# Optimization experiments

Hardware: AMD Instinct MI355X
Metric: run time of the kernel (lower is better)

## Reference

```python
import jax, jax.numpy as jnp
import numpy as np
from jax import lax

B, C, H, W = 4, 192, 64, 64
D_STATE, D_CONV, EXPAND = 16, 4, 2
D_INNER = EXPAND * C           # 384
DT_RANK = (C + 15) // 16       # 12 (mamba_ssm default ceil(d_model/16))


def setup_inputs() -> dict:
    key = jax.random.key(0)
    ks = jax.random.split(key, 12)
    sc = lambda k, shape, s=0.02: (jax.random.normal(k, shape, jnp.float32) * s)
    x = jax.random.normal(ks[0], (B, C, H, W), jnp.float32)
    norm_w = jnp.ones((C,), jnp.float32)
    norm_b = jnp.zeros((C,), jnp.float32)
    in_proj_w = sc(ks[1], (2 * D_INNER, C))
    conv_w = sc(ks[2], (D_INNER, D_CONV), 0.1)
    conv_b = jnp.zeros((D_INNER,), jnp.float32)
    x_proj_w = sc(ks[3], (DT_RANK + 2 * D_STATE, D_INNER))
    dt_proj_w = sc(ks[4], (D_INNER, DT_RANK), 0.1)
    # dt bias init so softplus(dt_bias) is in a realistic [1e-3, 1e-1] range
    dt0 = jax.random.uniform(ks[5], (D_INNER,), jnp.float32, 0.001, 0.1)
    dt_proj_b = jnp.log(jnp.expm1(dt0))
    A_log = jnp.log(jnp.broadcast_to(
        jnp.arange(1, D_STATE + 1, dtype=jnp.float32), (D_INNER, D_STATE)))
    D = jnp.ones((D_INNER,), jnp.float32)
    out_proj_w = sc(ks[6], (C, D_INNER))
    return {"x": x, "norm_w": norm_w, "norm_b": norm_b, "in_proj_w": in_proj_w,
            "conv_w": conv_w, "conv_b": conv_b, "x_proj_w": x_proj_w,
            "dt_proj_w": dt_proj_w, "dt_proj_b": dt_proj_b, "A_log": A_log,
            "D": D, "out_proj_w": out_proj_w}


def _mamba2d(x, norm_w, norm_b, in_proj_w, conv_w, conv_b, x_proj_w,
             dt_proj_w, dt_proj_b, A_log, D, out_proj_w):
    b, c, h, w = x.shape
    L = h * w
    seq = x.reshape(b, c, L).transpose(0, 2, 1)            # (B, L, C)
    # LayerNorm over channel dim
    mu = seq.mean(-1, keepdims=True)
    var = ((seq - mu) ** 2).mean(-1, keepdims=True)
    seqn = (seq - mu) * lax.rsqrt(var + 1e-5) * norm_w + norm_b
    # in_proj -> (x, z)
    xz = seqn @ in_proj_w.T                                # (B, L, 2*d_inner)
    xin, z = jnp.split(xz, 2, axis=-1)
    # causal depthwise conv1d over L
    xc = xin.transpose(0, 2, 1)                            # (B, d_inner, L)
    xc = lax.conv_general_dilated(xc, conv_w[:, None, :], (1,),
                                  [(D_CONV - 1, 0)],
                                  feature_group_count=D_INNER)
    xc = jax.nn.silu(xc + conv_b[None, :, None])
    xs = xc.transpose(0, 2, 1)                             # (B, L, d_inner)
    # input-dependent dt, B, C
    dbl = xs @ x_proj_w.T                                  # (B, L, dt_rank+2n)
    dt = dbl[..., :DT_RANK]
    Bm = dbl[..., DT_RANK:DT_RANK + D_STATE]               # (B, L, n)
    Cm = dbl[..., DT_RANK + D_STATE:]                      # (B, L, n)
    dt = jax.nn.softplus(dt @ dt_proj_w.T + dt_proj_b)     # (B, L, d_inner)
    A = -jnp.exp(A_log)                                    # (d_inner, n)
    dA = jnp.exp(dt[..., None] * A)                        # (B, L, d_inner, n)
    dBx = jnp.einsum('bld,bln->bldn', dt * xs, Bm)         # (B, L, d_inner, n)
    # selective scan over L
    def step(hcar, inp):
        dA_t, dBx_t, C_t = inp
        hcar = dA_t * hcar + dBx_t                         # (B, d_inner, n)
        y_t = jnp.einsum('bdn,bn->bd', hcar, C_t)
        return hcar, y_t
    h0 = jnp.zeros((b, D_INNER, D_STATE), xs.dtype)
    _, ys = lax.scan(step, h0, (jnp.moveaxis(dA, 1, 0),
                                jnp.moveaxis(dBx, 1, 0),
                                jnp.moveaxis(Cm, 1, 0)))
    y = jnp.moveaxis(ys, 0, 1) + xs * D                    # (B, L, d_inner)
    y = y * jax.nn.silu(z)
    out = y @ out_proj_w.T                                 # (B, L, C)
    return x + out.transpose(0, 2, 1).reshape(b, c, h, w)


def reference(x, norm_w, norm_b, in_proj_w, conv_w, conv_b, x_proj_w,
              dt_proj_w, dt_proj_b, A_log, D, out_proj_w):
    return _mamba2d(x, norm_w, norm_b, in_proj_w, conv_w, conv_b, x_proj_w,
                    dt_proj_w, dt_proj_b, A_log, D, out_proj_w)
```

## Files before the change

kernel.cpp:

```cpp
#include <hip/hip_runtime.h>
#include <hip/hip_bf16.h>

constexpr int B_ = 4;
constexpr int C_ = 192;
constexpr int L_ = 4096;
constexpr int DI = 384;
constexpr int DSs = 16;
constexpr int DTR = 12;
constexpr int NDBL = 44;
constexpr int NCHUNK = 128;
constexpr int CSZ = 32;
constexpr int NSUP = 8;

constexpr size_t BL = (size_t)B_ * L_;

constexpr size_t F_SEQN = 0;
constexpr size_t F_XIN  = F_SEQN + BL * C_ / 2;
constexpr size_t F_Z    = F_XIN + BL * DI / 2;
constexpr size_t F_XSB  = F_Z + BL * DI / 2;
constexpr size_t F_DBL  = F_XSB + BL * DI / 2;
constexpr size_t F_DT   = F_DBL + BL * NDBL;
constexpr size_t F_SBUF = F_DT + BL * DI / 2;
constexpr size_t F_HLOC = F_SBUF + (size_t)B_ * NCHUNK * DI;
constexpr size_t F_SPRE = F_HLOC + (size_t)B_ * NCHUNK * DI * 16 / 2;
constexpr size_t F_HSUP = F_SPRE + (size_t)B_ * NCHUNK * DI;
constexpr size_t F_SSUP = F_HSUP + (size_t)B_ * NSUP * 16 * DI;
constexpr size_t F_ISUP = F_SSUP + (size_t)B_ * NSUP * DI;
constexpr size_t F_WBUF = F_ISUP + (size_t)B_ * NSUP * 16 * DI;

typedef __attribute__((ext_vector_type(8))) short bf16x8;
typedef __attribute__((ext_vector_type(4))) float f32x4;

__device__ __forceinline__ unsigned short f2bf(float v) {
  unsigned x = __builtin_bit_cast(unsigned, v);
  unsigned r = x + 0x7FFFu + ((x >> 16) & 1u);
  return (unsigned short)(r >> 16);
}
__device__ __forceinline__ float bf2f(unsigned short u) {
  return __builtin_bit_cast(float, (unsigned)u << 16);
}
__device__ __forceinline__ void gload16(const void* g, void* l) {
  __builtin_amdgcn_global_load_lds((const __attribute__((address_space(1))) void*)g,
                                   (__attribute__((address_space(3))) void*)l, 16, 0, 0);
}
#define MFMA16(a, b, c) __builtin_amdgcn_mfma_f32_16x16x32_bf16(a, b, c, 0, 0, 0)

__global__ __launch_bounds__(256) void k_ln(const float* __restrict__ x,
                                            const float* __restrict__ nw,
                                            const float* __restrict__ nb,
                                            unsigned short* __restrict__ seqn,
                                            const float* __restrict__ ipw,
                                            const float* __restrict__ xpw,
                                            const float* __restrict__ opw,
                                            unsigned short* __restrict__ wbuf) {
  if (blockIdx.x >= 1024) {
    int t = (blockIdx.x - 1024) * 256 + threadIdx.x;
    if (t < 239616) {
      float v;
      if (t < 147456) v = ipw[t];
      else if (t < 165888) {
        int j = t - 147456;
        int r = j / 384, c = j - r * 384;
        v = (r < 44) ? xpw[r * 384 + c] : 0.f;
      } else v = opw[t - 165888];
      wbuf[t] = f2bf(v);
    }
    return;
  }
  __shared__ unsigned short xt[192][18];
  __shared__ float ps[16][16], ps2[16][16];
  __shared__ float mu_[16], rs_[16];
  __shared__ float wsh[192], bsh[192];
  int tid = threadIdx.x;
  int blk = blockIdx.x;
  int b = blk >> 8;
  int l0 = (blk & 255) << 4;
  const float* xb = x + (size_t)b * C_ * L_;
  for (int idx = tid; idx < 192 * 4; idx += 256) {
    int c = idx >> 2, lq = idx & 3;
    float4 v = *(const float4*)&xb[(size_t)c * L_ + l0 + (lq << 2)];
    ushort2 u0, u1;
    u0.x = f2bf(v.x); u0.y = f2bf(v.y);
    u1.x = f2bf(v.z); u1.y = f2bf(v.w);
    *(ushort2*)&xt[c][(lq << 2)] = u0;
    *(ushort2*)&xt[c][(lq << 2) + 2] = u1;
  }
  if (tid < 192) { wsh[tid] = nw[tid]; bsh[tid] = nb[tid]; }
  __syncthreads();
  int ll = tid & 15, q = tid >> 4;
  float s = 0.f, ss = 0.f;
  for (int c = q * 12; c < q * 12 + 12; ++c) {
    float v = bf2f(xt[c][ll]);
    s += v; ss += v * v;
  }
  ps[q][ll] = s; ps2[q][ll] = ss;
  __syncthreads();
  if (q == 0) {
    float st = 0.f, sst = 0.f;
#pragma unroll
    for (int g = 0; g < 16; ++g) { st += ps[g][ll]; sst += ps2[g][ll]; }
    float mu = st * (1.f / 192.f);
    float var = sst * (1.f / 192.f) - mu * mu;
    mu_[ll] = mu; rs_[ll] = rsqrtf(var + 1e-5f);
  }
  __syncthreads();
  unsigned short* so = seqn + ((size_t)b * L_ + l0) * C_;
  for (int idx = tid; idx < 16 * 192; idx += 256) {
    int l = idx / 192, c = idx - l * 192;
    so[idx] = f2bf((bf2f(xt[c][l]) - mu_[l]) * rs_[l] * wsh[c] + bsh[c]);
  }
}

__global__ __launch_bounds__(256) void k_inproj(const unsigned short* __restrict__ A,
                                                const unsigned short* __restrict__ W,
                                                unsigned short* __restrict__ xin,
                                                unsigned short* __restrict__ z) {
  __shared__ unsigned short smem[16384];
  unsigned short* As = smem;
  unsigned short* Bs = smem + 8192;
  int tid = threadIdx.x;
  int w = tid >> 6, l = tid & 63;
  int wr = w >> 1, wc = w & 1;
  int m0 = blockIdx.x << 7;
  int n0 = blockIdx.y << 7;
  f32x4 acc[4][4];
#pragma unroll
  for (int i = 0; i < 4; ++i)
#pragma unroll
    for (int j = 0; j < 4; ++j) acc[i][j] = (f32x4){0.f, 0.f, 0.f, 0.f};
  int lr = l & 15, lk = l >> 4;
  for (int kt = 0; kt < 3; ++kt) {
    int k0 = kt * 64;
    if (kt) __syncthreads();
#pragma unroll
    for (int i = 0; i < 4; ++i) {
      int row = (i << 5) + (tid >> 3);
      int gc = k0 + (((tid & 7) ^ (row & 7)) << 3);
      gload16(A + (size_t)(m0 + row) * 192 + gc, &As[(i << 11) + (w << 9)]);
      gload16(W + (size_t)(n0 + row) * 192 + gc, &Bs[(i << 11) + (w << 9)]);
    }
    __syncthreads();
#pragma unroll
    for (int ks = 0; ks < 2; ++ks) {
      int s = (ks << 2) + lk;
      bf16x8 af[4], bfr[4];
#pragma unroll
      for (int mi = 0; mi < 4; ++mi) {
        int r = (wr << 6) + (mi << 4) + lr;
        af[mi] = *(const bf16x8*)&As[r * 64 + ((s ^ (r & 7)) << 3)];
      }
#pragma unroll
      for (int ni = 0; ni < 4; ++ni) {
        int r = (wc << 6) + (ni << 4) + lr;
        bfr[ni] = *(const bf16x8*)&Bs[r * 64 + ((s ^ (r & 7)) << 3)];
      }
#pragma unroll
      for (int mi = 0; mi < 4; ++mi)
#pragma unroll
        for (int ni = 0; ni < 4; ++ni) acc[mi][ni] = MFMA16(af[mi], bfr[ni], acc[mi][ni]);
    }
  }
  __syncthreads();
#pragma unroll
  for (int mi = 0; mi < 4; ++mi)
#pragma unroll
    for (int ni = 0; ni < 4; ++ni) {
      int col = (wc << 6) + (ni << 4) + lr;
#pragma unroll
      for (int r = 0; r < 4; ++r) {
        int row = (wr << 6) + (mi << 4) + (lk << 2) + r;
        smem[(row << 7) + col] = f2bf(acc[mi][ni][r]);
      }
    }
  __syncthreads();
#pragma unroll
  for (int i = 0; i < 8; ++i) {
    int chunk = i * 256 + tid;
    int row = chunk >> 4, cq = chunk & 15;
    int n = n0 + (cq << 3);
    unsigned short* dst = (n < 384) ? (xin + (size_t)(m0 + row) * DI + n)
                                    : (z + (size_t)(m0 + row) * DI + (n - 384));
    *(bf16x8*)dst = *(const bf16x8*)&smem[(row << 7) + (cq << 3)];
  }
}

__global__ __launch_bounds__(384) void k_convx(const unsigned short* __restrict__ xin,
                                               const float* __restrict__ cw,
                                               const float* __restrict__ cb,
                                               const unsigned short* __restrict__ W,
                                               const float* __restrict__ dw,
                                               const float* __restrict__ dbias,
                                               const float* __restrict__ A_log,
                                               unsigned short* __restrict__ xsb,
                                               float* __restrict__ dbl,
                                               unsigned short* __restrict__ dtb,
                                               unsigned short* __restrict__ Hloc,
                                               float* __restrict__ Sbuf) {
  __shared__ unsigned short xs[6 * 2048];
  __shared__ unsigned short Bs[2][3072];
  __shared__ float dl[CSZ][12];
  __shared__ float Bsh2[CSZ][16];
  int tid = threadIdx.x;
  int w = tid >> 6, l = tid & 63;
  int b = blockIdx.y;
  int chunk = blockIdx.x;
  int l0 = chunk << 5;
  int d = tid;
  float4 w4 = *(const float4*)&cw[d * 4];
  float bb = cb[d];
  const unsigned short* xp = xin + ((size_t)b * L_ + l0) * DI + d;
  unsigned short* op = xsb + ((size_t)b * L_ + l0) * DI + d;
  float x0 = 0.f, x1 = 0.f, x2 = 0.f;
  if (l0 > 0) {
    x0 = bf2f(*(xp - 3 * DI));
    x1 = bf2f(*(xp - 2 * DI));
    x2 = bf2f(*(xp - DI));
  }
  int kt = d >> 6, col = d & 63, g = col >> 3, e = col & 7;
  unsigned short* xsrow = xs + kt * 2048;
  for (int r = 0; r < 32; ++r) {
    float xv = bf2f(xp[(size_t)r * DI]);
    float a = bb + w4.x * x0 + w4.y * x1 + w4.z * x2 + w4.w * xv;
    float sv = a * __builtin_amdgcn_rcpf(1.f + __expf(-a));
    unsigned short sb = f2bf(sv);
    xsrow[r * 64 + ((g ^ (r & 7)) << 3) + e] = sb;
    op[(size_t)r * DI] = sb;
    x0 = x1; x1 = x2; x2 = xv;
  }
  __syncthreads();
  int lr = l & 15, lk = l >> 4;
  int mt = w & 1, nt = w >> 1;
  {
    int row = tid >> 3;
    int gc = (((tid & 7) ^ (row & 7)) << 3);
    gload16(W + (size_t)row * 384 + gc, &Bs[0][w << 9]);
  }
  f32x4 accx = (f32x4){0.f, 0.f, 0.f, 0.f};
  for (int kt2 = 0; kt2 < 6; ++kt2) {
    __syncthreads();
    if (kt2 < 5) {
      int k0 = (kt2 + 1) * 64;
      int row = tid >> 3;
      int gc = k0 + (((tid & 7) ^ (row & 7)) << 3);
      gload16(W + (size_t)row * 384 + gc, &Bs[(kt2 + 1) & 1][w << 9]);
    }
    const unsigned short* Bcur = Bs[kt2 & 1];
#pragma unroll
    for (int ks = 0; ks < 2; ++ks) {
      int s = (ks << 2) + lk;
      int ar = (mt << 4) + lr;
      bf16x8 a = *(const bf16x8*)&xs[kt2 * 2048 + ar * 64 + ((s ^ (ar & 7)) << 3)];
      int br = (nt << 4) + lr;
      bf16x8 bbv = *(const bf16x8*)&Bcur[br * 64 + ((s ^ (br & 7)) << 3)];
      accx = MFMA16(a, bbv, accx);
    }
  }
  {
    int colq = (nt << 4) + lr;
#pragma unroll
    for (int r = 0; r < 4; ++r) {
      int row = (mt << 4) + (lk << 2) + r;
      float v = accx[r];
      if (colq < NDBL) dbl[((size_t)b * L_ + l0 + row) * NDBL + colq] = v;
      if (colq < 12) dl[row][colq] = v;
      else if (colq < 28) Bsh2[row][colq - 12] = v;
    }
  }
  __syncthreads();
  float4 wv0 = *(const float4*)&dw[d * 12];
  float4 wv1 = *(const float4*)&dw[d * 12 + 4];
  float4 wv2 = *(const float4*)&dw[d * 12 + 8];
  float bias = dbias[d];
  bool fast = true;
#pragma unroll
  for (int n = 0; n < 16; ++n) {
    float An_ = -__expf(A_log[d * 16 + n]);
    fast = fast && (fabsf(An_ + (float)(n + 1)) < 2e-3f);
  }
  unsigned short* dtp = dtb + ((size_t)b * L_ + l0) * DI + d;
  float h[16];
#pragma unroll
  for (int n = 0; n < 16; ++n) h[n] = 0.f;
  float S = 0.f;
  if (fast) {
#pragma unroll
    for (int i = 0; i < CSZ; ++i) {
      float4 c0 = *(const float4*)&dl[i][0];
      float4 c1 = *(const float4*)&dl[i][4];
      float4 c2 = *(const float4*)&dl[i][8];
      float a = bias;
      a = fmaf(wv0.x, c0.x, a); a = fmaf(wv0.y, c0.y, a);
      a = fmaf(wv0.z, c0.z, a); a = fmaf(wv0.w, c0.w, a);
      a = fmaf(wv1.x, c1.x, a); a = fmaf(wv1.y, c1.y, a);
      a = fmaf(wv1.z, c1.z, a); a = fmaf(wv1.w, c1.w, a);
      a = fmaf(wv2.x, c2.x, a); a = fmaf(wv2.y, c2.y, a);
      a = fmaf(wv2.z, c2.z, a); a = fmaf(wv2.w, c2.w, a);
      float sp = fmaxf(a, 0.f) + __logf(1.f + __expf(-fabsf(a)));
      dtp[(size_t)i * DI] = f2bf(sp);
      S += sp;
      float xv = bf2f(xsrow[i * 64 + ((g ^ (i & 7)) << 3) + e]);
      float dtx = sp * xv;
      float r = __expf(-sp);
      float r2 = r * r;
      float r4 = r2 * r2;
      float dA0 = r, dA1 = r2, dA2 = r2 * r, dA3 = r4;
#pragma unroll
      for (int gg = 0; gg < 4; ++gg) {
        float4 Bg = *(const float4*)&Bsh2[i][gg << 2];
        h[(gg << 2) + 0] = fmaf(dA0, h[(gg << 2) + 0], dtx * Bg.x);
        h[(gg << 2) + 1] = fmaf(dA1, h[(gg << 2) + 1], dtx * Bg.y);
        h[(gg << 2) + 2] = fmaf(dA2, h[(gg << 2) + 2], dtx * Bg.z);
        h[(gg << 2) + 3] = fmaf(dA3, h[(gg << 2) + 3], dtx * Bg.w);
        if (gg < 3) { dA0 *= r4; dA1 *= r4; dA2 *= r4; dA3 *= r4; }
      }
    }
  } else {
    float An[16];
#pragma unroll
    for (int n = 0; n < 16; ++n) An[n] = -__expf(A_log[d * 16 + n]);
#pragma unroll
    for (int i = 0; i < CSZ; ++i) {
      float4 c0 = *(const float4*)&dl[i][0];
      float4 c1 = *(const float4*)&dl[i][4];
      float4 c2 = *(const float4*)&dl[i][8];
      float a = bias;
      a = fmaf(wv0.x, c0.x, a); a = fmaf(wv0.y, c0.y, a);
      a = fmaf(wv0.z, c0.z, a); a = fmaf(wv0.w, c0.w, a);
      a = fmaf(wv1.x, c1.x, a); a = fmaf(wv1.y, c1.y, a);
      a = fmaf(wv1.z, c1.z, a); a = fmaf(wv1.w, c1.w, a);
      a = fmaf(wv2.x, c2.x, a); a = fmaf(wv2.y, c2.y, a);
      a = fmaf(wv2.z, c2.z, a); a = fmaf(wv2.w, c2.w, a);
      float sp = fmaxf(a, 0.f) + __logf(1.f + __expf(-fabsf(a)));
      dtp[(size_t)i * DI] = f2bf(sp);
      S += sp;
      float xv = bf2f(xsrow[i * 64 + ((g ^ (i & 7)) << 3) + e]);
      float dtx = sp * xv;
#pragma unroll
      for (int n = 0; n < 16; ++n)
        h[n] = fmaf(__expf(sp * An[n]), h[n], dtx * Bsh2[i][n]);
    }
  }
  size_t hbase = ((size_t)(b * NCHUNK + chunk) * 16) * DI + d;
#pragma unroll
  for (int n = 0; n < 16; ++n) Hloc[hbase + (size_t)n * DI] = f2bf(h[n]);
  Sbuf[((size_t)b * NCHUNK + chunk) * DI + d] = S;
}

__global__ __launch_bounds__(384) void k_scanB1(const float* __restrict__ A_log,
                                                unsigned short* __restrict__ Hloc,
                                                const float* __restrict__ Sbuf,
                                                float* __restrict__ Spre,
                                                float* __restrict__ Hsup,
                                                float* __restrict__ Ssup) {
  int d = threadIdx.x;
  int blk = blockIdx.x;
  int n = blk & 15;
  int s = (blk >> 4) & 7;
  int b = blk >> 7;
  float An = -__expf(A_log[d * 16 + n]);
  float h = 0.f, Sp = 0.f;
  int c0 = s * 16;
#pragma unroll
  for (int i = 0; i < 16; ++i) {
    int c = c0 + i;
    size_t hidx = (((size_t)(b * NCHUNK + c) * 16) + n) * DI + d;
    float Hl = bf2f(Hloc[hidx]);
    float S = Sbuf[((size_t)b * NCHUNK + c) * DI + d];
    Hloc[hidx] = f2bf(h);
    if (n == 0) Spre[((size_t)b * NCHUNK + c) * DI + d] = Sp;
    h = fmaf(__expf(An * S), h, Hl);
    Sp += S;
  }
  Hsup[(((size_t)(b * NSUP + s) * 16) + n) * DI + d] = h;
  if (n == 0) Ssup[((size_t)b * NSUP + s) * DI + d] = Sp;
}

__global__ __launch_bounds__(384) void k_scanC(const unsigned short* __restrict__ xsb,
                                               const unsigned short* __restrict__ dtb,
                                               const float* __restrict__ dbl,
                                               const unsigned short* __restrict__ z,
                                               const float* __restrict__ A_log,
                                               const float* __restrict__ Dw,
                                               const unsigned short* __restrict__ Hloc,
                                               const float* __restrict__ Spre,
                                               const float* __restrict__ Hsup,
                                               const float* __restrict__ Ssup,
                                               const unsigned short* __restrict__ Wo,
                                               const float* __restrict__ x,
                                               float* __restrict__ out) {
  __shared__ float BCsh[CSZ][32];
  __shared__ unsigned short yt[6 * 2048];
  __shared__ unsigned short Bs[12288];
  int tid = threadIdx.x;
  int blk = blockIdx.x;
  int b = blk >> 7;
  int chunk = blk & (NCHUNK - 1);
  int l0 = chunk << 5;
  int w = tid >> 6, l = tid & 63;
#pragma unroll
  for (int j = 0; j < 4; ++j) {
    int row = j * 48 + (tid >> 3);
    int gc = (((tid & 7) ^ (row & 7)) << 3);
    gload16(Wo + (size_t)row * 384 + gc, &Bs[j * 3072 + (w << 9)]);
  }
  for (int idx = tid; idx < CSZ * 32; idx += 384) {
    int r = idx >> 5, n32 = idx & 31;
    BCsh[r][n32] = dbl[((size_t)b * L_ + l0 + r) * NDBL + DTR + n32];
  }
  int d = tid;
  float Dd = Dw[d];
  bool fast = true;
#pragma unroll
  for (int n = 0; n < 16; ++n) {
    float An_ = -__expf(A_log[d * 16 + n]);
    fast = fast && (fabsf(An_ + (float)(n + 1)) < 2e-3f);
  }
  int sup = chunk >> 4;
  size_t hbase = ((size_t)(b * NCHUNK + chunk) * 16) * DI + d;
  float Spv = Spre[((size_t)b * NCHUNK + chunk) * DI + d];
  float h[16];
  if (fast) {
    float I[16];
#pragma unroll
    for (int n = 0; n < 16; ++n) I[n] = 0.f;
    for (int s = 0; s < sup; ++s) {
      float Ss = Ssup[((size_t)b * NSUP + s) * DI + d];
      const float* Hs = Hsup + ((size_t)(b * NSUP + s) * 16) * DI + d;
      float t = __expf(-Ss);
      float t2 = t * t, t4 = t2 * t2;
      float p0 = t, p1 = t2, p2 = t2 * t, p3 = t4;
#pragma unroll
      for (int gI = 0; gI < 4; ++gI) {
        I[(gI << 2) + 0] = fmaf(p0, I[(gI << 2) + 0], Hs[(size_t)((gI << 2) + 0) * DI]);
        I[(gI << 2) + 1] = fmaf(p1, I[(gI << 2) + 1], Hs[(size_t)((gI << 2) + 1) * DI]);
        I[(gI << 2) + 2] = fmaf(p2, I[(gI << 2) + 2], Hs[(size_t)((gI << 2) + 2) * DI]);
        I[(gI << 2) + 3] = fmaf(p3, I[(gI << 2) + 3], Hs[(size_t)((gI << 2) + 3) * DI]);
        if (gI < 3) { p0 *= t4; p1 *= t4; p2 *= t4; p3 *= t4; }
      }
    }
    float t = __expf(-Spv);
    float t2 = t * t, t4 = t2 * t2;
    float p0 = t, p1 = t2, p2 = t2 * t, p3 = t4;
#pragma unroll
    for (int gI = 0; gI < 4; ++gI) {
      h[(gI << 2) + 0] = fmaf(p0, I[(gI << 2) + 0], bf2f(Hloc[hbase + (size_t)((gI << 2) + 0) * DI]));
      h[(gI << 2) + 1] = fmaf(p1, I[(gI << 2) + 1], bf2f(Hloc[hbase + (size_t)((gI << 2) + 1) * DI]));
      h[(gI << 2) + 2] = fmaf(p2, I[(gI << 2) + 2], bf2f(Hloc[hbase + (size_t)((gI << 2) + 2) * DI]));
      h[(gI << 2) + 3] = fmaf(p3, I[(gI << 2) + 3], bf2f(Hloc[hbase + (size_t)((gI << 2) + 3) * DI]));
      if (gI < 3) { p0 *= t4; p1 *= t4; p2 *= t4; p3 *= t4; }
    }
  } else {
    float An[16];
#pragma unroll
    for (int n = 0; n < 16; ++n) An[n] = -__expf(A_log[d * 16 + n]);
    float I[16];
#pragma unroll
    for (int n = 0; n < 16; ++n) I[n] = 0.f;
    for (int s = 0; s < sup; ++s) {
      float Ss = Ssup[((size_t)b * NSUP + s) * DI + d];
      const float* Hs = Hsup + ((size_t)(b * NSUP + s) * 16) * DI + d;
#pragma unroll
      for (int n = 0; n < 16; ++n)
        I[n] = fmaf(__expf(An[n] * Ss), I[n], Hs[(size_t)n * DI]);
    }
#pragma unroll
    for (int n = 0; n < 16; ++n)
      h[n] = fmaf(__expf(An[n] * Spv), I[n], bf2f(Hloc[hbase + (size_t)n * DI]));
  }
  const unsigned short* xp = xsb + ((size_t)b * L_ + l0) * DI + d;
  const unsigned short* dtp = dtb + ((size_t)b * L_ + l0) * DI + d;
  const unsigned short* zp = z + ((size_t)b * L_ + l0) * DI + d;
  int ktile = d >> 6, colq = d & 63, gq = colq >> 3, eq = colq & 7;
  unsigned short* ytp = yt + ktile * 2048;
  __syncthreads();
  if (fast) {
#pragma unroll
    for (int i = 0; i < CSZ; ++i) {
      float sp = bf2f(dtp[(size_t)i * DI]);
      float xv = bf2f(xp[(size_t)i * DI]);
      float zv = bf2f(zp[(size_t)i * DI]);
      float dtx = sp * xv;
      float r = __expf(-sp);
      float r2 = r * r;
      float r4 = r2 * r2;
      float dA0 = r, dA1 = r2, dA2 = r2 * r, dA3 = r4;
      float y = 0.f;
#pragma unroll
      for (int g = 0; g < 4; ++g) {
        float4 Bg = *(const float4*)&BCsh[i][g << 2];
        float4 Cg = *(const float4*)&BCsh[i][16 + (g << 2)];
        h[(g << 2) + 0] = fmaf(dA0, h[(g << 2) + 0], dtx * Bg.x);
        h[(g << 2) + 1] = fmaf(dA1, h[(g << 2) + 1], dtx * Bg.y);
        h[(g << 2) + 2] = fmaf(dA2, h[(g << 2) + 2], dtx * Bg.z);
        h[(g << 2) + 3] = fmaf(dA3, h[(g << 2) + 3], dtx * Bg.w);
        y = fmaf(h[(g << 2) + 0], Cg.x, y);
        y = fmaf(h[(g << 2) + 1], Cg.y, y);
        y = fmaf(h[(g << 2) + 2], Cg.z, y);
        y = fmaf(h[(g << 2) + 3], Cg.w, y);
        if (g < 3) { dA0 *= r4; dA1 *= r4; dA2 *= r4; dA3 *= r4; }
      }
      y = fmaf(xv, Dd, y);
      float sig = __builtin_amdgcn_rcpf(1.f + __expf(-zv));
      ytp[i * 64 + ((gq ^ (i & 7)) << 3) + eq] = f2bf(y * (zv * sig));
    }
  } else {
    float An[16];
#pragma unroll
    for (int n = 0; n < 16; ++n) An[n] = -__expf(A_log[d * 16 + n]);
#pragma unroll
    for (int i = 0; i < CSZ; ++i) {
      float sp = bf2f(dtp[(size_t)i * DI]);
      float xv = bf2f(xp[(size_t)i * DI]);
      float zv = bf2f(zp[(size_t)i * DI]);
      float dtx = sp * xv;
      float y = 0.f;
#pragma unroll
      for (int n = 0; n < 16; ++n) {
        h[n] = fmaf(__expf(sp * An[n]), h[n], dtx * BCsh[i][n]);
        y = fmaf(h[n], BCsh[i][16 + n], y);
      }
      y = fmaf(xv, Dd, y);
      float sig = __builtin_amdgcn_rcpf(1.f + __expf(-zv));
      ytp[i * 64 + ((gq ^ (i & 7)) << 3) + eq] = f2bf(y * (zv * sig));
    }
  }
  int lr = l & 15, lk = l >> 4;
  int mt = w & 1;
  int ng = w >> 1;
  f32x4 acc[4];
#pragma unroll
  for (int j = 0; j < 4; ++j) acc[j] = (f32x4){0.f, 0.f, 0.f, 0.f};
  for (int kt = 0; kt < 6; ++kt) {
    __syncthreads();
#pragma unroll
    for (int ks = 0; ks < 2; ++ks) {
      int s = (ks << 2) + lk;
      bf16x8 a = *(const bf16x8*)&yt[kt * 2048 + (mt * 16 + lr) * 64 + ((s ^ (lr & 7)) << 3)];
#pragma unroll
      for (int j = 0; j < 4; ++j) {
        int br = (ng * 4 + j) * 16 + lr;
        bf16x8 bv = *(const bf16x8*)&Bs[br * 64 + ((s ^ (br & 7)) << 3)];
        acc[j] = MFMA16(a, bv, acc[j]);
      }
    }
    if (kt < 5) {
      __syncthreads();
      int k0 = (kt + 1) * 64;
#pragma unroll
      for (int j = 0; j < 4; ++j) {
        int row = j * 48 + (tid >> 3);
        int gc = k0 + (((tid & 7) ^ (row & 7)) << 3);
        gload16(Wo + (size_t)row * 384 + gc, &Bs[j * 3072 + (w << 9)]);
      }
    }
  }
#pragma unroll
  for (int j = 0; j < 4; ++j) {
    int c = (ng * 4 + j) * 16 + lr;
    size_t off = ((size_t)b * C_ + c) * L_ + l0 + mt * 16 + (lk << 2);
    f32x4 xv = *(const f32x4*)&x[off];
    *(f32x4*)&out[off] = acc[j] + xv;
  }
}

extern "C" void kernel_launch(void* const* d_in, const int* in_sizes, int n_in,
                              void* d_out, int out_size, void* d_ws, size_t ws_size,
                              hipStream_t stream) {
  const float* x         = (const float*)d_in[0];
  const float* norm_w    = (const float*)d_in[1];
  const float* norm_b    = (const float*)d_in[2];
  const float* in_proj_w = (const float*)d_in[3];
  const float* conv_w    = (const float*)d_in[4];
  const float* conv_b    = (const float*)d_in[5];
  const float* x_proj_w  = (const float*)d_in[6];
  const float* dt_proj_w = (const float*)d_in[7];
  const float* dt_proj_b = (const float*)d_in[8];
  const float* A_log     = (const float*)d_in[9];
  const float* Dw        = (const float*)d_in[10];
  const float* out_proj_w= (const float*)d_in[11];
  float* out = (float*)d_out;
  float* ws = (float*)d_ws;

  unsigned short* seqn = (unsigned short*)(ws + F_SEQN);
  unsigned short* xin  = (unsigned short*)(ws + F_XIN);
  unsigned short* z    = (unsigned short*)(ws + F_Z);
  unsigned short* xsb  = (unsigned short*)(ws + F_XSB);
  float* dbl           = ws + F_DBL;
  unsigned short* dtb  = (unsigned short*)(ws + F_DT);
  float* Sbuf          = ws + F_SBUF;
  unsigned short* Hloc = (unsigned short*)(ws + F_HLOC);
  float* Spre          = ws + F_SPRE;
  float* Hsup          = ws + F_HSUP;
  float* Ssup          = ws + F_SSUP;
  unsigned short* wbuf = (unsigned short*)(ws + F_WBUF);
  unsigned short* ipw  = wbuf;
  unsigned short* xpw  = wbuf + 147456;
  unsigned short* opw  = wbuf + 165888;

  hipLaunchKernelGGL(k_ln, dim3(1960), dim3(256), 0, stream, x, norm_w, norm_b, seqn,
                     in_proj_w, x_proj_w, out_proj_w, wbuf);
  hipLaunchKernelGGL(k_inproj, dim3(128, 6), dim3(256), 0, stream, seqn, ipw, xin, z);
  hipLaunchKernelGGL(k_convx, dim3(128, 4), dim3(384), 0, stream, xin, conv_w, conv_b, xpw,
                     dt_proj_w, dt_proj_b, A_log, xsb, dbl, dtb, Hloc, Sbuf);
  hipLaunchKernelGGL(k_scanB1, dim3(512), dim3(384), 0, stream, A_log, Hloc, Sbuf, Spre, Hsup,
                     Ssup);
  hipLaunchKernelGGL(k_scanC, dim3(512), dim3(384), 0, stream, xsb, dtb, dbl, z, A_log, Dw,
                     Hloc, Spre, Hsup, Ssup, opw, x, out);
}
```

Measured before the change: 96.53 us.

## Fuse conv, x_proj, chunk scan and out_proj into one cooperative kernel

Replaces the three launches for conv/x_proj, the inter-chunk scan and the output pass with a single cooperative kernel that uses grid-wide syncs between phases. The conv output, dt values and B/C projections stay in registers and LDS across phases, so the xsb/dbl/dtb round trips through global memory and two launch gaps go away. In exchange it needs 512 blocks of 384 threads to be co-resident (it checks occupancy and falls back to the old path), grid.sync carries its own cost, and LDS and register pressure rise.

```diff
diff --git a/kernel.cpp b/kernel.cpp
--- a/kernel.cpp
+++ b/kernel.cpp
@@ -1,5 +1,6 @@
 #include <hip/hip_runtime.h>
 #include <hip/hip_bf16.h>
+#include <hip/hip_cooperative_groups.h>
 
 constexpr int B_ = 4;
 constexpr int C_ = 192;
@@ -25,8 +26,7 @@
 constexpr size_t F_SPRE = F_HLOC + (size_t)B_ * NCHUNK * DI * 16 / 2;
 constexpr size_t F_HSUP = F_SPRE + (size_t)B_ * NCHUNK * DI;
 constexpr size_t F_SSUP = F_HSUP + (size_t)B_ * NSUP * 16 * DI;
-constexpr size_t F_ISUP = F_SSUP + (size_t)B_ * NSUP * DI;
-constexpr size_t F_WBUF = F_ISUP + (size_t)B_ * NSUP * 16 * DI;
+constexpr size_t F_WBUF = F_SSUP + (size_t)B_ * NSUP * DI;
 
 typedef __attribute__((ext_vector_type(8))) short bf16x8;
 typedef __attribute__((ext_vector_type(4))) float f32x4;
@@ -563,6 +563,360 @@
   }
 }
 
+__global__ __launch_bounds__(384) void k_mega(const unsigned short* __restrict__ xin,
+                                              const float* __restrict__ cw,
+                                              const float* __restrict__ cb,
+                                              const unsigned short* __restrict__ W,
+                                              const float* __restrict__ dw,
+                                              const float* __restrict__ dbias,
+                                              const float* __restrict__ A_log,
+                                              const float* __restrict__ Dw,
+                                              unsigned short* __restrict__ Hloc,
+                                              float* __restrict__ Sbuf,
+                                              float* __restrict__ Spre,
+                                              float* __restrict__ Hsup,
+                                              float* __restrict__ Ssup,
+                                              const unsigned short* __restrict__ z,
+                                              const unsigned short* __restrict__ Wo,
+                                              const float* __restrict__ x,
+                                              float* __restrict__ out) {
+  __shared__ unsigned short xsyt[6 * 2048];
+  __shared__ unsigned short BsW[12288];
+  __shared__ float bc[CSZ][44];
+  namespace cg = cooperative_groups;
+  cg::grid_group grid = cg::this_grid();
+  int tid = threadIdx.x;
+  int bid = blockIdx.x;
+  int b = bid >> 7;
+  int chunk = bid & 127;
+  int l0 = chunk << 5;
+  int d = tid;
+  int w = tid >> 6, l = tid & 63;
+  int lr = l & 15, lk = l >> 4;
+  int ktA = d >> 6, colA = d & 63, g = colA >> 3, e = colA & 7;
+  unsigned dtpk[16];
+
+  {
+    float4 w4 = *(const float4*)&cw[d * 4];
+    float bb = cb[d];
+    const unsigned short* xp = xin + ((size_t)b * L_ + l0) * DI + d;
+    float x0 = 0.f, x1 = 0.f, x2 = 0.f;
+    if (l0 > 0) {
+      x0 = bf2f(*(xp - 3 * DI));
+      x1 = bf2f(*(xp - 2 * DI));
+      x2 = bf2f(*(xp - DI));
+    }
+    unsigned short* xsrow = xsyt + ktA * 2048;
+#pragma unroll
+    for (int r = 0; r < 32; ++r) {
+      float xv = bf2f(xp[(size_t)r * DI]);
+      float a = bb + w4.x * x0 + w4.y * x1 + w4.z * x2 + w4.w * xv;
+      float sv = a * __builtin_amdgcn_rcpf(1.f + __expf(-a));
+      xsrow[r * 64 + ((g ^ (r & 7)) << 3) + e] = f2bf(sv);
+      x0 = x1; x1 = x2; x2 = xv;
+    }
+  }
+  __syncthreads();
+  int mt = w & 1, nt = w >> 1;
+  {
+    int row = tid >> 3;
+    int gc = (((tid & 7) ^ (row & 7)) << 3);
+    gload16(W + (size_t)row * 384 + gc, &BsW[w << 9]);
+  }
+  f32x4 accx = (f32x4){0.f, 0.f, 0.f, 0.f};
+  for (int kt2 = 0; kt2 < 6; ++kt2) {
+    __syncthreads();
+    if (kt2 < 5) {
+      int k0 = (kt2 + 1) * 64;
+      int row = tid >> 3;
+      int gc = k0 + (((tid & 7) ^ (row & 7)) << 3);
+      gload16(W + (size_t)row * 384 + gc, &BsW[((kt2 + 1) & 1) * 3072 + (w << 9)]);
+    }
+    const unsigned short* Bcur = BsW + (kt2 & 1) * 3072;
+#pragma unroll
+    for (int ks = 0; ks < 2; ++ks) {
+      int s = (ks << 2) + lk;
+      int ar = (mt << 4) + lr;
+      bf16x8 a = *(const bf16x8*)&xsyt[kt2 * 2048 + ar * 64 + ((s ^ (ar & 7)) << 3)];
+      int br = (nt << 4) + lr;
+      bf16x8 bbv = *(const bf16x8*)&Bcur[br * 64 + ((s ^ (br & 7)) << 3)];
+      accx = MFMA16(a, bbv, accx);
+    }
+  }
+  {
+    int colq = (nt << 4) + lr;
+#pragma unroll
+    for (int r = 0; r < 4; ++r) {
+      int row = (mt << 4) + (lk << 2) + r;
+      if (colq < NDBL) bc[row][colq] = accx[r];
+    }
+  }
+  __syncthreads();
+  bool fast = true;
+#pragma unroll
+  for (int n = 0; n < 16; ++n) {
+    float An_ = -__expf(A_log[d * 16 + n]);
+    fast = fast && (fabsf(An_ + (float)(n + 1)) < 2e-3f);
+  }
+  float h[16];
+#pragma unroll
+  for (int n = 0; n < 16; ++n) h[n] = 0.f;
+  {
+    float4 wv0 = *(const float4*)&dw[d * 12];
+    float4 wv1 = *(const float4*)&dw[d * 12 + 4];
+    float4 wv2 = *(const float4*)&dw[d * 12 + 8];
+    float bias = dbias[d];
+    const unsigned short* xsrow = xsyt + ktA * 2048;
+    float S = 0.f;
+    if (fast) {
+#pragma unroll
+      for (int i = 0; i < CSZ; ++i) {
+        float4 c0 = *(const float4*)&bc[i][0];
+        float4 c1 = *(const float4*)&bc[i][4];
+        float4 c2 = *(const float4*)&bc[i][8];
+        float a = bias;
+        a = fmaf(wv0.x, c0.x, a); a = fmaf(wv0.y, c0.y, a);
+        a = fmaf(wv0.z, c0.z, a); a = fmaf(wv0.w, c0.w, a);
+        a = fmaf(wv1.x, c1.x, a); a = fmaf(wv1.y, c1.y, a);
+        a = fmaf(wv1.z, c1.z, a); a = fmaf(wv1.w, c1.w, a);
+        a = fmaf(wv2.x, c2.x, a); a = fmaf(wv2.y, c2.y, a);
+        a = fmaf(wv2.z, c2.z, a); a = fmaf(wv2.w, c2.w, a);
+        float sp = fmaxf(a, 0.f) + __logf(1.f + __expf(-fabsf(a)));
+        unsigned short su = f2bf(sp);
+        if ((i & 1) == 0) dtpk[i >> 1] = (unsigned)su;
+        else dtpk[i >> 1] |= ((unsigned)su) << 16;
+        S += sp;
+        float xv = bf2f(xsrow[i * 64 + ((g ^ (i & 7)) << 3) + e]);
+        float dtx = sp * xv;
+        float r = __expf(-sp);
+        float r2 = r * r;
+        float r4 = r2 * r2;
+        float dA0 = r, dA1 = r2, dA2 = r2 * r, dA3 = r4;
+#pragma unroll
+        for (int gg = 0; gg < 4; ++gg) {
+          float4 Bg = *(const float4*)&bc[i][12 + (gg << 2)];
+          h[(gg << 2) + 0] = fmaf(dA0, h[(gg << 2) + 0], dtx * Bg.x);
+          h[(gg << 2) + 1] = fmaf(dA1, h[(gg << 2) + 1], dtx * Bg.y);
+          h[(gg << 2) + 2] = fmaf(dA2, h[(gg << 2) + 2], dtx * Bg.z);
+          h[(gg << 2) + 3] = fmaf(dA3, h[(gg << 2) + 3], dtx * Bg.w);
+          if (gg < 3) { dA0 *= r4; dA1 *= r4; dA2 *= r4; dA3 *= r4; }
+        }
+      }
+    } else {
+      float An[16];
+#pragma unroll
+      for (int n = 0; n < 16; ++n) An[n] = -__expf(A_log[d * 16 + n]);
+#pragma unroll
+      for (int i = 0; i < CSZ; ++i) {
+        float4 c0 = *(const float4*)&bc[i][0];
+        float4 c1 = *(const float4*)&bc[i][4];
+        float4 c2 = *(const float4*)&bc[i][8];
+        float a = bias;
+        a = fmaf(wv0.x, c0.x, a); a = fmaf(wv0.y, c0.y, a);
+        a = fmaf(wv0.z, c0.z, a); a = fmaf(wv0.w, c0.w, a);
+        a = fmaf(wv1.x, c1.x, a); a = fmaf(wv1.y, c1.y, a);
+        a = fmaf(wv1.z, c1.z, a); a = fmaf(wv1.w, c1.w, a);
+        a = fmaf(wv2.x, c2.x, a); a = fmaf(wv2.y, c2.y, a);
+        a = fmaf(wv2.z, c2.z, a); a = fmaf(wv2.w, c2.w, a);
+        float sp = fmaxf(a, 0.f) + __logf(1.f + __expf(-fabsf(a)));
+        unsigned short su = f2bf(sp);
+        if ((i & 1) == 0) dtpk[i >> 1] = (unsigned)su;
+        else dtpk[i >> 1] |= ((unsigned)su) << 16;
+        S += sp;
+        float xv = bf2f(xsrow[i * 64 + ((g ^ (i & 7)) << 3) + e]);
+        float dtx = sp * xv;
+#pragma unroll
+        for (int n = 0; n < 16; ++n)
+          h[n] = fmaf(__expf(sp * An[n]), h[n], dtx * bc[i][12 + n]);
+      }
+    }
+    size_t hbase = ((size_t)(b * NCHUNK + chunk) * 16) * DI + d;
+#pragma unroll
+    for (int n = 0; n < 16; ++n) Hloc[hbase + (size_t)n * DI] = f2bf(h[n]);
+    Sbuf[((size_t)b * NCHUNK + chunk) * DI + d] = S;
+  }
+  grid.sync();
+  {
+    int n2 = bid & 15;
+    int s2 = (bid >> 4) & 7;
+    int b2 = bid >> 7;
+    float An = -__expf(A_log[d * 16 + n2]);
+    float hh = 0.f, Sp = 0.f;
+    int c0 = s2 * 16;
+#pragma unroll
+    for (int i = 0; i < 16; ++i) {
+      int c = c0 + i;
+      size_t hidx = (((size_t)(b2 * NCHUNK + c) * 16) + n2) * DI + d;
+      float Hl = bf2f(Hloc[hidx]);
+      float Sv = Sbuf[((size_t)b2 * NCHUNK + c) * DI + d];
+      Hloc[hidx] = f2bf(hh);
+      if (n2 == 0) Spre[((size_t)b2 * NCHUNK + c) * DI + d] = Sp;
+      hh = fmaf(__expf(An * Sv), hh, Hl);
+      Sp += Sv;
+    }
+    Hsup[(((size_t)(b2 * NSUP + s2) * 16) + n2) * DI + d] = hh;
+    if (n2 == 0) Ssup[((size_t)b2 * NSUP + s2) * DI + d] = Sp;
+  }
+  grid.sync();
+#pragma unroll
+  for (int j = 0; j < 4; ++j) {
+    int row = j * 48 + (tid >> 3);
+    int gc = (((tid & 7) ^ (row & 7)) << 3);
+    gload16(Wo + (size_t)row * 384 + gc, &BsW[j * 3072 + (w << 9)]);
+  }
+  float Dd = Dw[d];
+  int sup = chunk >> 4;
+  size_t hbase = ((size_t)(b * NCHUNK + chunk) * 16) * DI + d;
+  float Spv = Spre[((size_t)b * NCHUNK + chunk) * DI + d];
+  if (fast) {
+    float I[16];
+#pragma unroll
+    for (int n = 0; n < 16; ++n) I[n] = 0.f;
+    for (int s = 0; s < sup; ++s) {
+      float Ss = Ssup[((size_t)b * NSUP + s) * DI + d];
+      const float* Hs = Hsup + ((size_t)(b * NSUP + s) * 16) * DI + d;
+      float t = __expf(-Ss);
+      float t2 = t * t, t4 = t2 * t2;
+      float p0 = t, p1 = t2, p2 = t2 * t, p3 = t4;
+#pragma unroll
+      for (int gI = 0; gI < 4; ++gI) {
+        I[(gI << 2) + 0] = fmaf(p0, I[(gI << 2) + 0], Hs[(size_t)((gI << 2) + 0) * DI]);
+        I[(gI << 2) + 1] = fmaf(p1, I[(gI << 2) + 1], Hs[(size_t)((gI << 2) + 1) * DI]);
+        I[(gI << 2) + 2] = fmaf(p2, I[(gI << 2) + 2], Hs[(size_t)((gI << 2) + 2) * DI]);
+        I[(gI << 2) + 3] = fmaf(p3, I[(gI << 2) + 3], Hs[(size_t)((gI << 2) + 3) * DI]);
+        if (gI < 3) { p0 *= t4; p1 *= t4; p2 *= t4; p3 *= t4; }
+      }
+    }
+    float t = __expf(-Spv);
+    float t2 = t * t, t4 = t2 * t2;
+    float p0 = t, p1 = t2, p2 = t2 * t, p3 = t4;
+#pragma unroll
+    for (int gI = 0; gI < 4; ++gI) {
+      h[(gI << 2) + 0] = fmaf(p0, I[(gI << 2) + 0], bf2f(Hloc[hbase + (size_t)((gI << 2) + 0) * DI]));
+      h[(gI << 2) + 1] = fmaf(p1, I[(gI << 2) + 1], bf2f(Hloc[hbase + (size_t)((gI << 2) + 1) * DI]));
+      h[(gI << 2) + 2] = fmaf(p2, I[(gI << 2) + 2], bf2f(Hloc[hbase + (size_t)((gI << 2) + 2) * DI]));
+      h[(gI << 2) + 3] = fmaf(p3, I[(gI << 2) + 3], bf2f(Hloc[hbase + (size_t)((gI << 2) + 3) * DI]));
+      if (gI < 3) { p0 *= t4; p1 *= t4; p2 *= t4; p3 *= t4; }
+    }
+  } else {
+    float An[16];
+#pragma unroll
+    for (int n = 0; n < 16; ++n) An[n] = -__expf(A_log[d * 16 + n]);
+    float I[16];
+#pragma unroll
+    for (int n = 0; n < 16; ++n) I[n] = 0.f;
+    for (int s = 0; s < sup; ++s) {
+      float Ss = Ssup[((size_t)b * NSUP + s) * DI + d];
+      const float* Hs = Hsup + ((size_t)(b * NSUP + s) * 16) * DI + d;
+#pragma unroll
+      for (int n = 0; n < 16; ++n)
+        I[n] = fmaf(__expf(An[n] * Ss), I[n], Hs[(size_t)n * DI]);
+    }
+#pragma unroll
+    for (int n = 0; n < 16; ++n)
+      h[n] = fmaf(__expf(An[n] * Spv), I[n], bf2f(Hloc[hbase + (size_t)n * DI]));
+  }
+  {
+    const unsigned short* zp = z + ((size_t)b * L_ + l0) * DI + d;
+    unsigned short* ytp = xsyt + ktA * 2048;
+    if (fast) {
+#pragma unroll
+      for (int i = 0; i < CSZ; ++i) {
+        unsigned short du = (i & 1) ? (unsigned short)(dtpk[i >> 1] >> 16)
+                                    : (unsigned short)(dtpk[i >> 1] & 0xFFFFu);
+        int slot = i * 64 + ((g ^ (i & 7)) << 3) + e;
+        float sp = bf2f(du);
+        float xv = bf2f(ytp[slot]);
+        float zv = bf2f(zp[(size_t)i * DI]);
+        float dtx = sp * xv;
+        float r = __expf(-sp);
+        float r2 = r * r;
+        float r4 = r2 * r2;
+        float dA0 = r, dA1 = r2, dA2 = r2 * r, dA3 = r4;
+        float y = 0.f;
+#pragma unroll
+        for (int gg = 0; gg < 4; ++gg) {
+          float4 Bg = *(const float4*)&bc[i][12 + (gg << 2)];
+          float4 Cg = *(const float4*)&bc[i][28 + (gg << 2)];
+          h[(gg << 2) + 0] = fmaf(dA0, h[(gg << 2) + 0], dtx * Bg.x);
+          h[(gg << 2) + 1] = fmaf(dA1, h[(gg << 2) + 1], dtx * Bg.y);
+          h[(gg << 2) + 2] = fmaf(dA2, h[(gg << 2) + 2], dtx * Bg.z);
+          h[(gg << 2) + 3] = fmaf(dA3, h[(gg << 2) + 3], dtx * Bg.w);
+          y = fmaf(h[(gg << 2) + 0], Cg.x, y);
+          y = fmaf(h[(gg << 2) + 1], Cg.y, y);
+          y = fmaf(h[(gg << 2) + 2], Cg.z, y);
+          y = fmaf(h[(gg << 2) + 3], Cg.w, y);
+          if (gg < 3) { dA0 *= r4; dA1 *= r4; dA2 *= r4; dA3 *= r4; }
+        }
+        y = fmaf(xv, Dd, y);
+        float sig = __builtin_amdgcn_rcpf(1.f + __expf(-zv));
+        ytp[slot] = f2bf(y * (zv * sig));
+      }
+    } else {
+      float An[16];
+#pragma unroll
+      for (int n = 0; n < 16; ++n) An[n] = -__expf(A_log[d * 16 + n]);
+#pragma unroll
+      for (int i = 0; i < CSZ; ++i) {
+        unsigned short du = (i & 1) ? (unsigned short)(dtpk[i >> 1] >> 16)
+                                    : (unsigned short)(dtpk[i >> 1] & 0xFFFFu);
+        int slot = i * 64 + ((g ^ (i & 7)) << 3) + e;
+        float sp = bf2f(du);
+        float xv = bf2f(ytp[slot]);
+        float zv = bf2f(zp[(size_t)i * DI]);
+        float dtx = sp * xv;
+        float y = 0.f;
+#pragma unroll
+        for (int n = 0; n < 16; ++n) {
+          h[n] = fmaf(__expf(sp * An[n]), h[n], dtx * bc[i][12 + n]);
+          y = fmaf(h[n], bc[i][28 + n], y);
+        }
+        y = fmaf(xv, Dd, y);
+        float sig = __builtin_amdgcn_rcpf(1.f + __expf(-zv));
+        ytp[slot] = f2bf(y * (zv * sig));
+      }
+    }
+  }
+  {
+    int mt2 = w & 1;
+    int ng = w >> 1;
+    f32x4 acc[4];
+#pragma unroll
+    for (int j = 0; j < 4; ++j) acc[j] = (f32x4){0.f, 0.f, 0.f, 0.f};
+    for (int kt = 0; kt < 6; ++kt) {
+      __syncthreads();
+#pragma unroll
+      for (int ks = 0; ks < 2; ++ks) {
+        int s = (ks << 2) + lk;
+        bf16x8 a = *(const bf16x8*)&xsyt[kt * 2048 + (mt2 * 16 + lr) * 64 + ((s ^ (lr & 7)) << 3)];
+#pragma unroll
+        for (int j = 0; j < 4; ++j) {
+          int br = (ng * 4 + j) * 16 + lr;
+          bf16x8 bv = *(const bf16x8*)&BsW[br * 64 + ((s ^ (br & 7)) << 3)];
+          acc[j] = MFMA16(a, bv, acc[j]);
+        }
+      }
+      if (kt < 5) {
+        __syncthreads();
+        int k0 = (kt + 1) * 64;
+#pragma unroll
+        for (int j = 0; j < 4; ++j) {
+          int row = j * 48 + (tid >> 3);
+          int gc = k0 + (((tid & 7) ^ (row & 7)) << 3);
+          gload16(Wo + (size_t)row * 384 + gc, &BsW[j * 3072 + (w << 9)]);
+        }
+      }
+    }
+#pragma unroll
+    for (int j = 0; j < 4; ++j) {
+      int c = (ng * 4 + j) * 16 + lr;
+      size_t off = ((size_t)b * C_ + c) * L_ + l0 + mt2 * 16 + (lk << 2);
+      f32x4 xv = *(const f32x4*)&x[off];
+      *(f32x4*)&out[off] = acc[j] + xv;
+    }
+  }
+}
+
 extern "C" void kernel_launch(void* const* d_in, const int* in_sizes, int n_in,
                               void* d_out, int out_size, void* d_ws, size_t ws_size,
                               hipStream_t stream) {
@@ -600,10 +954,23 @@
   hipLaunchKernelGGL(k_ln, dim3(1960), dim3(256), 0, stream, x, norm_w, norm_b, seqn,
                      in_proj_w, x_proj_w, out_proj_w, wbuf);
   hipLaunchKernelGGL(k_inproj, dim3(128, 6), dim3(256), 0, stream, seqn, ipw, xin, z);
-  hipLaunchKernelGGL(k_convx, dim3(128, 4), dim3(384), 0, stream, xin, conv_w, conv_b, xpw,
-                     dt_proj_w, dt_proj_b, A_log, xsb, dbl, dtb, Hloc, Sbuf);
-  hipLaunchKernelGGL(k_scanB1, dim3(512), dim3(384), 0, stream, A_log, Hloc, Sbuf, Spre, Hsup,
-                     Ssup);
-  hipLaunchKernelGGL(k_scanC, dim3(512), dim3(384), 0, stream, xsb, dtb, dbl, z, A_log, Dw,
-                     Hloc, Spre, Hsup, Ssup, opw, x, out);
+
+  int maxb = 0;
+  hipError_t oe = hipOccupancyMaxActiveBlocksPerMultiprocessor(&maxb, k_mega, 384, 0);
+  bool useMega = (oe == hipSuccess) && (maxb >= 2);
+
+  if (useMega) {
+    void* margs[] = {(void*)&xin, (void*)&conv_w, (void*)&conv_b, (void*)&xpw,
+                     (void*)&dt_proj_w, (void*)&dt_proj_b, (void*)&A_log, (void*)&Dw,
+                     (void*)&Hloc, (void*)&Sbuf, (void*)&Spre, (void*)&Hsup, (void*)&Ssup,
+                     (void*)&z, (void*)&opw, (void*)&x, (void*)&out};
+    hipLaunchCooperativeKernel((void*)k_mega, dim3(512), dim3(384), margs, 0, stream);
+  } else {
+    hipLaunchKernelGGL(k_convx, dim3(128, 4), dim3(384), 0, stream, xin, conv_w, conv_b, xpw,
+                       dt_proj_w, dt_proj_b, A_log, xsb, dbl, dtb, Hloc, Sbuf);
+    hipLaunchKernelGGL(k_scanB1, dim3(512), dim3(384), 0, stream, A_log, Hloc, Sbuf, Spre, Hsup,
+                       Ssup);
+    hipLaunchKernelGGL(k_scanC, dim3(512), dim3(384), 0, stream, xsb, dtb, dbl, z, A_log, Dw,
+                       Hloc, Spre, Hsup, Ssup, opw, x, out);
+  }
 }
```

New measurement: 96.43 us. No clear change (-0.1%).
